# Kernel optimization log

Hardware: AMD Instinct MI355X
Metric: run time of the kernel (lower is better)

## Reference

```python
import jax, jax.numpy as jnp
import numpy as np

S = 2048
HIDDEN = 4096
NH, NKV, HD = 32, 8, 128
QPK = NH // NKV  # 4
BLOCK, LOCAL, VERT = 64, 16, 8
ROPE_BASE = 1.0e6
SCALE = 1.0 / HD  # mup scaling: head_dim / mup_attn_multiplier(=1.0)


def setup_inputs() -> dict:
    key = jax.random.key(0)
    ks = jax.random.split(key, 5)
    qkv_out = NKV * (QPK + 2) * HD  # 6144, head-major layout
    return {
        "positions": jnp.arange(S, dtype=jnp.int32),
        "hidden_states": jax.random.normal(ks[0], (S, HIDDEN), jnp.float32),
        "w_qkv": jax.random.normal(ks[1], (qkv_out, HIDDEN), jnp.float32) * 0.02,
        "b_qkv": jax.random.normal(ks[2], (qkv_out,), jnp.float32) * 0.02,
        "w_dense": jax.random.normal(ks[3], (HIDDEN, HIDDEN), jnp.float32) * 0.02,
        "b_dense": jax.random.normal(ks[4], (HIDDEN,), jnp.float32) * 0.02,
    }


def _rope(x, cos, sin):
    # NeoX-style (non-interleaved) rotary over full head_dim.
    # x: [S, n_heads, HD]; cos/sin: [S, HD//2]
    d2 = x.shape[-1] // 2
    x1, x2 = x[..., :d2], x[..., d2:]
    c, s = cos[:, None, :], sin[:, None, :]
    return jnp.concatenate([x1 * c - x2 * s, x2 * c + x1 * s], axis=-1)


def _blocksparse_mask(positions):
    # vllm phi3small pattern: block (qb,kb) active iff causal AND
    # (qb-kb < local_blocks OR (kb + head + 1) % vert_stride == 0), hetero heads.
    qb = positions // BLOCK                       # [S]
    heads = jnp.arange(NH, dtype=positions.dtype)
    diff = qb[:, None] - qb[None, :]              # [S,S]
    local = diff < LOCAL                          # [S,S]
    vert = ((qb[None, None, :] + heads[:, None, None] + 1) % VERT) == 0  # [NH,1,S]
    causal = positions[:, None] >= positions[None, :]                     # [S,S]
    return (local[None] | vert) & causal[None]    # [NH,S,S]


def reference(positions, hidden_states, w_qkv, b_qkv, w_dense, b_dense):
    seq = hidden_states.shape[0]
    qkv = hidden_states @ w_qkv.T + b_qkv                   # [S, 6144]
    qkv = qkv.reshape(seq, NKV, QPK + 2, HD)                # head-major split
    q = qkv[:, :, :QPK].reshape(seq, NH, HD)
    k = qkv[:, :, QPK]                                      # [S, NKV, HD]
    v = qkv[:, :, QPK + 1]

    pos = positions.astype(jnp.float32)  # rope_position_scale = 1.0
    inv_freq = 1.0 / (ROPE_BASE ** (jnp.arange(0, HD, 2, dtype=jnp.float32) / HD))
    freqs = pos[:, None] * inv_freq                          # [S, HD/2]
    cos, sin = jnp.cos(freqs), jnp.sin(freqs)
    q = _rope(q, cos, sin)
    k = _rope(k, cos, sin)

    # GQA: each kv head serves QPK query heads
    kx = jnp.repeat(k, QPK, axis=1)                          # [S, NH, HD]
    vx = jnp.repeat(v, QPK, axis=1)

    scores = jnp.einsum('qhd,khd->hqk', q, kx) * SCALE       # [NH,S,S]
    mask = _blocksparse_mask(positions)
    scores = jnp.where(mask, scores, -jnp.inf)  # diag always in local block -> no empty rows
    p = jax.nn.softmax(scores, axis=-1)
    out = jnp.einsum('hqk,khd->qhd', p, vx).reshape(seq, NH * HD)
    return out @ w_dense.T + b_dense
```

## Files before the change

### kernel.cpp

```cpp
#include <hip/hip_runtime.h>

#define S_LEN   2048
#define HID     4096
#define NHEADS  32
#define NKVH    8
#define HDIM    128
#define NQKV    6144
#define ATT_SCALE (1.0f/128.0f)

typedef unsigned short u16;
typedef __attribute__((ext_vector_type(8))) __bf16 bf16x8;
typedef __attribute__((ext_vector_type(4))) float  f32x4;

__device__ __forceinline__ u16 f2bf(float f) {
    union { float f; unsigned u; } x; x.f = f;
    unsigned u = x.u;
    u += 0x7fffu + ((u >> 16) & 1u);
    return (u16)(u >> 16);
}
__device__ __forceinline__ float bf2f(u16 v) {
    union { unsigned u; float f; } x; x.u = ((unsigned)v) << 16; return x.f;
}

__global__ __launch_bounds__(256) void cvt_bf16_kernel(const float* __restrict__ in,
                                                       u16* __restrict__ out, int n4) {
    int stride = gridDim.x * blockDim.x;
    for (int i = blockIdx.x * blockDim.x + threadIdx.x; i < n4; i += stride) {
        float4 v = *(const float4*)(in + (size_t)i * 4);
        ushort4 o = make_ushort4(f2bf(v.x), f2bf(v.y), f2bf(v.z), f2bf(v.w));
        *(ushort4*)(out + (size_t)i * 4) = o;
    }
}

#define GFENCE() asm volatile("" ::: "memory")
#define GSBAR()  do { GFENCE(); __builtin_amdgcn_s_barrier(); GFENCE(); } while (0)

template <int BN_, int NB_, bool OUT_BF16>
__global__ __launch_bounds__(512, 2) void gemm_fc_kernel(
    const u16* __restrict__ A,
    const u16* __restrict__ B,
    const float* __restrict__ bias,
    void* __restrict__ Cout,
    int M, int N, int K)
{
    constexpr int LB = BN_ / 128;
    constexpr int VM = 2 + LB;
    __shared__ u16 lds[16384 + 2 * BN_ * 64];

    const int tid  = threadIdx.x;
    const int wid  = tid >> 6;
    const int lane = tid & 63;
    const int ln   = lane & 15;
    const int quad = lane >> 4;
    const int wr   = wid >> 2;
    const int wc   = wid & 3;
    const int tileM = blockIdx.y * 128;
    const int tileN = blockIdx.x * BN_;

    f32x4 acc[2][NB_][4];
    #pragma unroll
    for (int b = 0; b < 2; b++)
        #pragma unroll
        for (int n = 0; n < NB_; n++)
            #pragma unroll
            for (int m = 0; m < 4; m++) {
                f32x4 z = {0.f, 0.f, 0.f, 0.f};
                acc[b][n][m] = z;
            }

    const int srho = lane >> 3;
    const int scol = (((lane & 7) ^ srho) << 3);

    auto gload = [&](const u16* src, u16* dst) {
        __builtin_amdgcn_global_load_lds(
            (const __attribute__((address_space(1))) void*)src,
            (__attribute__((address_space(3))) void*)dst, 16, 0, 0);
    };
    auto stage_A = [&](int kk, int bb) {
        const int base = bb * 8192;
        #pragma unroll
        for (int s = 0; s < 2; s++) {
            const int rho0 = s * 64 + wid * 8;
            const int rho  = rho0 + srho;
            const u16* src = A + (size_t)(tileM + rho) * K + (size_t)kk * 64 + scol;
            gload(src, &lds[base + rho0 * 64]);
        }
    };
    auto stage_Bh = [&](int h, int kk, int bb) {
        const int base = 16384 + bb * (BN_ * 64) + h * ((BN_ / 2) * 64);
        #pragma unroll
        for (int s = 0; s < LB; s++) {
            const int rho0 = s * 64 + wid * 8;
            const int rho  = rho0 + srho;
            const u16* src = B + (size_t)(tileN + h * (BN_ / 2) + rho) * K
                               + (size_t)kk * 64 + scol;
            gload(src, &lds[base + rho0 * 64]);
        }
    };

#define WAIT_VM()                                                                   \
    do {                                                                            \
        if constexpr (VM == 5) asm volatile("s_waitcnt vmcnt(5)" ::: "memory");     \
        else                   asm volatile("s_waitcnt vmcnt(4)" ::: "memory");     \
    } while (0)

#define READ_A()                                                                    \
    do {                                                                            \
        _Pragma("unroll")                                                           \
        for (int m = 0; m < 4; m++) {                                               \
            const int ra = wr * 64 + m * 16 + ln;                                   \
            const int ab = buf * 8192 + ra * 64;                                    \
            const int rx = ra & 7;                                                  \
            af[m][0] = *(const bf16x8*)(&lds[ab + ((quad ^ rx) << 3)]);             \
            af[m][1] = *(const bf16x8*)(&lds[ab + (((4 + quad) ^ rx) << 3)]);       \
        }                                                                           \
    } while (0)

#define MFMA_B(b_)                                                                  \
    do {                                                                            \
        __builtin_amdgcn_s_setprio(1);                                              \
        _Pragma("unroll")                                                           \
        for (int n = 0; n < NB_; n++) {                                             \
            const int rb = (b_) * (BN_ / 2) + wc * (NB_ * 16) + n * 16 + ln;        \
            const int bb = 16384 + buf * (BN_ * 64) + rb * 64;                      \
            const int rx = rb & 7;                                                  \
            bf16x8 b0 = *(const bf16x8*)(&lds[bb + ((quad ^ rx) << 3)]);            \
            bf16x8 b1 = *(const bf16x8*)(&lds[bb + (((4 + quad) ^ rx) << 3)]);      \
            _Pragma("unroll")                                                       \
            for (int m = 0; m < 4; m++) {                                           \
                acc[b_][n][m] = __builtin_amdgcn_mfma_f32_16x16x32_bf16(            \
                    af[m][0], b0, acc[b_][n][m], 0, 0, 0);                          \
                acc[b_][n][m] = __builtin_amdgcn_mfma_f32_16x16x32_bf16(            \
                    af[m][1], b1, acc[b_][n][m], 0, 0, 0);                          \
            }                                                                       \
        }                                                                           \
        __builtin_amdgcn_s_setprio(0);                                              \
    } while (0)

    const int nIter = K / 64;

    stage_A(0, 0); stage_Bh(0, 0, 0); stage_Bh(1, 0, 0);

    bf16x8 af[4][2];

    for (int t = 0; t < nIter; t++) {
        const int buf = t & 1;
        const int bn  = buf ^ 1;
        const int kn  = (t + 1 == nIter) ? 0 : t + 1;

        stage_A(kn, bn);
        WAIT_VM();
        GSBAR();
        READ_A();
        MFMA_B(0);

        stage_Bh(0, kn, bn);
        WAIT_VM();
        GSBAR();
        MFMA_B(1);
        stage_Bh(1, kn, bn);

        asm volatile("s_waitcnt lgkmcnt(0)" ::: "memory");
        GSBAR();
    }

    asm volatile("s_waitcnt vmcnt(0)" ::: "memory");

#undef WAIT_VM
#undef READ_A
#undef MFMA_B

    #pragma unroll
    for (int b = 0; b < 2; b++)
        #pragma unroll
        for (int n = 0; n < NB_; n++) {
            const int col = tileN + b * (BN_ / 2) + wc * (NB_ * 16) + n * 16 + ln;
            const float bv = bias[col];
            #pragma unroll
            for (int m = 0; m < 4; m++) {
                #pragma unroll
                for (int r = 0; r < 4; r++) {
                    const int row = tileM + wr * 64 + m * 16 + quad * 4 + r;
                    float v = acc[b][n][m][r] + bv;
                    if (OUT_BF16)
                        ((u16*)Cout)[(size_t)row * N + col] = f2bf(v);
                    else
                        ((float*)Cout)[(size_t)row * N + col] = v;
                }
            }
        }
}

__global__ __launch_bounds__(128) void rope_split_kernel(
    const u16* __restrict__ qkv, const int* __restrict__ positions,
    u16* __restrict__ qb_o, u16* __restrict__ kb_o, u16* __restrict__ vb_o)
{
    const int d   = threadIdx.x;
    const int pos = blockIdx.x;
    const int hy  = blockIdx.y;
    const float p = (float)positions[pos];

    if (hy >= NHEADS + NKVH) {
        int kv = hy - NHEADS - NKVH;
        const u16* src = qkv + (size_t)pos * NQKV + (kv * 6 + 5) * HDIM;
        vb_o[((size_t)kv * S_LEN + pos) * HDIM + d] = src[d];
        return;
    }
    const u16* src;
    u16* dst;
    if (hy < NHEADS) {
        int kv = hy >> 2, qi = hy & 3;
        src = qkv + (size_t)pos * NQKV + (kv * 6 + qi) * HDIM;
        dst = qb_o + ((size_t)hy * S_LEN + pos) * HDIM;
    } else {
        int kv = hy - NHEADS;
        src = qkv + (size_t)pos * NQKV + (kv * 6 + 4) * HDIM;
        dst = kb_o + ((size_t)kv * S_LEN + pos) * HDIM;
    }
    int d2 = d & 63;
    float inv = expf(-(float)d2 * (13.815510557964274f / 64.0f));
    float fr = p * inv;
    float s, c;
    sincosf(fr, &s, &c);
    float x1 = bf2f(src[d2]);
    float x2 = bf2f(src[d2 + 64]);
    float o = (d < 64) ? (x1 * c - x2 * s) : (x2 * c + x1 * s);
    dst[d] = f2bf(o);
}

__global__ __launch_bounds__(256, 4) void attn_bs_kernel(
    const u16* __restrict__ Q,
    const u16* __restrict__ K,
    const u16* __restrict__ V,
    u16* __restrict__ O)
{
    __shared__ u16 Ks[64 * 128];
    __shared__ u16 Vt[128 * 64];
    __shared__ u16 Ps[4][16 * 64];

    const int qb = (int)gridDim.x - 1 - (int)blockIdx.x;
    const int h  = blockIdx.y;
    const int kv = h >> 2;
    const int tid  = threadIdx.x;
    const int w    = tid >> 6;
    const int lane = tid & 63;
    const int ln   = lane & 15;
    const int quad = lane >> 4;

    bf16x8 aq[4];
    {
        const u16* Qg = Q + ((size_t)h * S_LEN + qb * 64 + w * 16 + ln) * HDIM + quad * 8;
        #pragma unroll
        for (int ks = 0; ks < 4; ks++)
            aq[ks] = *(const bf16x8*)(Qg + ks * 32);
    }

    f32x4 oacc[8];
    #pragma unroll
    for (int n = 0; n < 8; n++) { f32x4 z = {0.f,0.f,0.f,0.f}; oacc[n] = z; }
    float mrow[4] = {-1e30f, -1e30f, -1e30f, -1e30f};
    float lrow[4] = {0.f, 0.f, 0.f, 0.f};

    for (int kb = 0; kb <= qb; kb++) {
        bool sel = (qb - kb < 16) || (((kb + h + 1) & 7) == 0);
        if (!sel) continue;

        __syncthreads();

        const u16* Kg = K + ((size_t)kv * S_LEN + kb * 64) * HDIM;
        const u16* Vg = V + ((size_t)kv * S_LEN + kb * 64) * HDIM;

        #pragma unroll
        for (int p = 0; p < 4; p++) {
            int r0  = w * 16 + p * 4;
            int row = r0 + (lane >> 4);
            const u16* src = Kg + (size_t)row * HDIM + (((lane & 15) ^ (row & 7)) << 3);
            __builtin_amdgcn_global_load_lds(
                (const __attribute__((address_space(1))) void*)src,
                (__attribute__((address_space(3))) void*)&Ks[r0 * 128], 16, 0, 0);
        }

        {
            int dbase = w * 32;
            #pragma unroll
            for (int p = 0; p < 4; p++) {
                int d0 = dbase + p * 8;
                uint4 vv = *(const uint4*)(Vg + (size_t)lane * HDIM + d0);
                const u16* pvv = (const u16*)&vv;
                #pragma unroll
                for (int jj = 0; jj < 8; jj++) {
                    int d = d0 + jj;
                    Vt[d * 64 + ((((lane >> 3)) ^ (d & 7)) << 3) + (lane & 7)] = pvv[jj];
                }
            }
        }
        __syncthreads();

        f32x4 sacc[4];
        #pragma unroll
        for (int jj = 0; jj < 4; jj++) { f32x4 z = {0.f,0.f,0.f,0.f}; sacc[jj] = z; }
        __builtin_amdgcn_s_setprio(1);
        #pragma unroll
        for (int ks = 0; ks < 4; ks++) {
            #pragma unroll
            for (int jj = 0; jj < 4; jj++) {
                bf16x8 bk = *(const bf16x8*)(
                    &Ks[(jj * 16 + ln) * 128 + (((ks * 4 + quad) ^ (ln & 7)) << 3)]);
                sacc[jj] = __builtin_amdgcn_mfma_f32_16x16x32_bf16(aq[ks], bk, sacc[jj], 0, 0, 0);
            }
        }
        __builtin_amdgcn_s_setprio(0);

        #pragma unroll
        for (int r = 0; r < 4; r++) {
            float pv[4];
            float mx = -1e30f;
            const int qrow = w * 16 + quad * 4 + r;
            #pragma unroll
            for (int jj = 0; jj < 4; jj++) {
                float s = sacc[jj][r] * ATT_SCALE;
                if (kb == qb && (jj * 16 + ln) > qrow) s = -1e30f;
                pv[jj] = s;
                mx = fmaxf(mx, s);
            }
            #pragma unroll
            for (int off = 1; off < 16; off <<= 1)
                mx = fmaxf(mx, __shfl_xor(mx, off, 64));
            float mnew  = fmaxf(mrow[r], mx);
            float alpha = __expf(mrow[r] - mnew);
            float sum = 0.f;
            #pragma unroll
            for (int jj = 0; jj < 4; jj++) {
                float pe = __expf(pv[jj] - mnew);
                pv[jj] = pe;
                sum += pe;
            }
            #pragma unroll
            for (int off = 1; off < 16; off <<= 1)
                sum += __shfl_xor(sum, off, 64);
            lrow[r] = lrow[r] * alpha + sum;
            mrow[r] = mnew;
            #pragma unroll
            for (int n = 0; n < 8; n++) oacc[n][r] *= alpha;
            const int prow = quad * 4 + r;
            #pragma unroll
            for (int jj = 0; jj < 4; jj++)
                Ps[w][prow * 64 + (((jj * 2 + (ln >> 3)) ^ (prow & 7)) << 3) + (ln & 7)]
                    = f2bf(pv[jj]);
        }

        __builtin_amdgcn_s_setprio(1);
        #pragma unroll
        for (int kk = 0; kk < 2; kk++) {
            bf16x8 ap = *(const bf16x8*)(
                &Ps[w][ln * 64 + (((kk * 4 + quad) ^ (ln & 7)) << 3)]);
            #pragma unroll
            for (int n = 0; n < 8; n++) {
                bf16x8 bv = *(const bf16x8*)(
                    &Vt[(n * 16 + ln) * 64 + (((kk * 4 + quad) ^ (ln & 7)) << 3)]);
                oacc[n] = __builtin_amdgcn_mfma_f32_16x16x32_bf16(ap, bv, oacc[n], 0, 0, 0);
            }
        }
        __builtin_amdgcn_s_setprio(0);
    }

    #pragma unroll
    for (int n = 0; n < 8; n++) {
        #pragma unroll
        for (int r = 0; r < 4; r++) {
            int row = w * 16 + quad * 4 + r;
            int pos = qb * 64 + row;
            float o = oacc[n][r] / lrow[r];
            O[(size_t)pos * (NHEADS * HDIM) + h * HDIM + n * 16 + ln] = f2bf(o);
        }
    }
}

extern "C" void kernel_launch(void* const* d_in, const int* in_sizes, int n_in,
                              void* d_out, int out_size, void* d_ws, size_t ws_size,
                              hipStream_t stream) {
    const int*   positions = (const int*)d_in[0];
    const float* hidden    = (const float*)d_in[1];
    const float* w_qkv     = (const float*)d_in[2];
    const float* b_qkv     = (const float*)d_in[3];
    const float* w_dense   = (const float*)d_in[4];
    const float* b_dense   = (const float*)d_in[5];
    float* out = (float*)d_out;

    char* ws = (char*)d_ws;
    u16* ws_h    = (u16*)(ws);
    u16* ws_wqkv = (u16*)(ws + 16777216);
    u16* ws_wd   = (u16*)(ws + 67108864);
    u16* ws_qkv  = (u16*)(ws + 100663296);
    u16* ws_q    = (u16*)(ws + 125829120);
    u16* ws_k    = (u16*)(ws + 142606336);
    u16* ws_v    = (u16*)(ws + 146800640);
    u16* ws_attn = (u16*)(ws + 150994944);

    cvt_bf16_kernel<<<1024, 256, 0, stream>>>(hidden,  ws_h,    (S_LEN * HID) / 4);
    cvt_bf16_kernel<<<2048, 256, 0, stream>>>(w_qkv,   ws_wqkv, (NQKV * HID) / 4);
    cvt_bf16_kernel<<<2048, 256, 0, stream>>>(w_dense, ws_wd,   (HID * HID) / 4);

    gemm_fc_kernel<384, 3, true><<<dim3(NQKV / 384, S_LEN / 128), 512, 0, stream>>>(
        ws_h, ws_wqkv, b_qkv, ws_qkv, S_LEN, NQKV, HID);

    rope_split_kernel<<<dim3(S_LEN, NHEADS + 2 * NKVH), 128, 0, stream>>>(
        ws_qkv, positions, ws_q, ws_k, ws_v);

    attn_bs_kernel<<<dim3(S_LEN / 64, NHEADS), 256, 0, stream>>>(ws_q, ws_k, ws_v, ws_attn);

    gemm_fc_kernel<256, 2, false><<<dim3(HID / 256, S_LEN / 128), 512, 0, stream>>>(
        ws_attn, ws_wd, b_dense, out, S_LEN, HID, HID);
}
```

Measured before the change: 520.9 us.

## Pre-transpose V globally and use lazy softmax rescaling in attention

After: 511.1 us. Within noise of the previous version (-1.9%).

```diff
diff --git a/kernel.cpp b/kernel.cpp
--- a/kernel.cpp
+++ b/kernel.cpp
@@ -193,19 +193,13 @@
 
 __global__ __launch_bounds__(128) void rope_split_kernel(
     const u16* __restrict__ qkv, const int* __restrict__ positions,
-    u16* __restrict__ qb_o, u16* __restrict__ kb_o, u16* __restrict__ vb_o)
+    u16* __restrict__ qb_o, u16* __restrict__ kb_o)
 {
     const int d   = threadIdx.x;
     const int pos = blockIdx.x;
     const int hy  = blockIdx.y;
     const float p = (float)positions[pos];
 
-    if (hy >= NHEADS + NKVH) {
-        int kv = hy - NHEADS - NKVH;
-        const u16* src = qkv + (size_t)pos * NQKV + (kv * 6 + 5) * HDIM;
-        vb_o[((size_t)kv * S_LEN + pos) * HDIM + d] = src[d];
-        return;
-    }
     const u16* src;
     u16* dst;
     if (hy < NHEADS) {
@@ -228,6 +222,33 @@
     dst[d] = f2bf(o);
 }
 
+__global__ __launch_bounds__(256) void vtrans_kernel(
+    const u16* __restrict__ qkv,
+    u16* __restrict__ VT)
+{
+    __shared__ u16 T[64][HDIM + 8];
+    const int s0 = blockIdx.x * 64;
+    const int kv = blockIdx.y;
+    const int tid = threadIdx.x;
+    #pragma unroll
+    for (int p = 0; p < 4; p++) {
+        int pos = p * 16 + (tid >> 4);
+        int d   = (tid & 15) * 8;
+        *(uint4*)&T[pos][d] =
+            *(const uint4*)(qkv + (size_t)(s0 + pos) * NQKV + (kv * 6 + 5) * HDIM + d);
+    }
+    __syncthreads();
+    #pragma unroll
+    for (int p = 0; p < 4; p++) {
+        int d  = p * 32 + (tid >> 3);
+        int sc = (tid & 7) * 8;
+        u16 tmp[8];
+        #pragma unroll
+        for (int j = 0; j < 8; j++) tmp[j] = T[sc + j][d];
+        *(uint4*)(VT + ((size_t)kv * HDIM + d) * S_LEN + s0 + sc) = *(uint4*)tmp;
+    }
+}
+
 __global__ __launch_bounds__(256, 4) void attn_bs_kernel(
     const u16* __restrict__ Q,
     const u16* __restrict__ K,
@@ -267,8 +288,8 @@
 
         __syncthreads();
 
-        const u16* Kg = K + ((size_t)kv * S_LEN + kb * 64) * HDIM;
-        const u16* Vg = V + ((size_t)kv * S_LEN + kb * 64) * HDIM;
+        const u16* Kg  = K + ((size_t)kv * S_LEN + kb * 64) * HDIM;
+        const u16* VTg = V + (size_t)kv * HDIM * S_LEN + kb * 64;
 
         #pragma unroll
         for (int p = 0; p < 4; p++) {
@@ -279,20 +300,15 @@
                 (const __attribute__((address_space(1))) void*)src,
                 (__attribute__((address_space(3))) void*)&Ks[r0 * 128], 16, 0, 0);
         }
-
-        {
-            int dbase = w * 32;
-            #pragma unroll
-            for (int p = 0; p < 4; p++) {
-                int d0 = dbase + p * 8;
-                uint4 vv = *(const uint4*)(Vg + (size_t)lane * HDIM + d0);
-                const u16* pvv = (const u16*)&vv;
-                #pragma unroll
-                for (int jj = 0; jj < 8; jj++) {
-                    int d = d0 + jj;
-                    Vt[d * 64 + ((((lane >> 3)) ^ (d & 7)) << 3) + (lane & 7)] = pvv[jj];
-                }
-            }
+        #pragma unroll
+        for (int p = 0; p < 4; p++) {
+            int r0  = w * 32 + p * 8;
+            int row = r0 + (lane >> 3);
+            int c   = (lane & 7) ^ (row & 7);
+            const u16* src = VTg + (size_t)row * S_LEN + c * 8;
+            __builtin_amdgcn_global_load_lds(
+                (const __attribute__((address_space(1))) void*)src,
+                (__attribute__((address_space(3))) void*)&Vt[r0 * 64], 16, 0, 0);
         }
         __syncthreads();
 
@@ -311,42 +327,55 @@
         }
         __builtin_amdgcn_s_setprio(0);
 
+        const bool diag = (kb == qb);
+        float pv[4][4], mxr[4];
+        bool grow = false;
         #pragma unroll
         for (int r = 0; r < 4; r++) {
-            float pv[4];
+            const int qrow = w * 16 + quad * 4 + r;
             float mx = -1e30f;
-            const int qrow = w * 16 + quad * 4 + r;
             #pragma unroll
             for (int jj = 0; jj < 4; jj++) {
                 float s = sacc[jj][r] * ATT_SCALE;
-                if (kb == qb && (jj * 16 + ln) > qrow) s = -1e30f;
-                pv[jj] = s;
+                if (diag && (jj * 16 + ln) > qrow) s = -1e30f;
+                pv[r][jj] = s;
                 mx = fmaxf(mx, s);
             }
             #pragma unroll
             for (int off = 1; off < 16; off <<= 1)
                 mx = fmaxf(mx, __shfl_xor(mx, off, 64));
-            float mnew  = fmaxf(mrow[r], mx);
-            float alpha = __expf(mrow[r] - mnew);
+            mxr[r] = mx;
+            grow |= (mx > mrow[r] + 8.0f);
+        }
+        if (__any(grow)) {
+            #pragma unroll
+            for (int r = 0; r < 4; r++) {
+                float mnew  = fmaxf(mrow[r], mxr[r]);
+                float alpha = __expf(mrow[r] - mnew);
+                lrow[r] *= alpha;
+                mrow[r]  = mnew;
+                #pragma unroll
+                for (int n = 0; n < 8; n++) oacc[n][r] *= alpha;
+            }
+        }
+        #pragma unroll
+        for (int r = 0; r < 4; r++) {
             float sum = 0.f;
             #pragma unroll
             for (int jj = 0; jj < 4; jj++) {
-                float pe = __expf(pv[jj] - mnew);
-                pv[jj] = pe;
+                float pe = __expf(pv[r][jj] - mrow[r]);
+                pv[r][jj] = pe;
                 sum += pe;
             }
             #pragma unroll
             for (int off = 1; off < 16; off <<= 1)
                 sum += __shfl_xor(sum, off, 64);
-            lrow[r] = lrow[r] * alpha + sum;
-            mrow[r] = mnew;
-            #pragma unroll
-            for (int n = 0; n < 8; n++) oacc[n][r] *= alpha;
+            lrow[r] += sum;
             const int prow = quad * 4 + r;
             #pragma unroll
             for (int jj = 0; jj < 4; jj++)
                 Ps[w][prow * 64 + (((jj * 2 + (ln >> 3)) ^ (prow & 7)) << 3) + (ln & 7)]
-                    = f2bf(pv[jj]);
+                    = f2bf(pv[r][jj]);
         }
 
         __builtin_amdgcn_s_setprio(1);
@@ -404,8 +433,10 @@
     gemm_fc_kernel<384, 3, true><<<dim3(NQKV / 384, S_LEN / 128), 512, 0, stream>>>(
         ws_h, ws_wqkv, b_qkv, ws_qkv, S_LEN, NQKV, HID);
 
-    rope_split_kernel<<<dim3(S_LEN, NHEADS + 2 * NKVH), 128, 0, stream>>>(
-        ws_qkv, positions, ws_q, ws_k, ws_v);
+    rope_split_kernel<<<dim3(S_LEN, NHEADS + NKVH), 128, 0, stream>>>(
+        ws_qkv, positions, ws_q, ws_k);
+
+    vtrans_kernel<<<dim3(S_LEN / 64, NKVH), 256, 0, stream>>>(ws_qkv, ws_v);
 
     attn_bs_kernel<<<dim3(S_LEN / 64, NHEADS), 256, 0, stream>>>(ws_q, ws_k, ws_v, ws_attn);
 
```
